# Performance work log

Measured on AMD Instinct MI355X. Metric: run time of the kernel, lower is better.

Reference implementation:

```python
import jax, jax.numpy as jnp
import numpy as np

B, T, D = 32, 128, 64
SPK, CELL, NCLS = 2, 64, 6
DIMS = [300, 74, 35]
BETA = 0.8            # QActivation beta
TWO_PI = 2 * 3.14     # repo uses 2*3.14, not 2*pi


def _unitary(seed, d):
    rng = np.random.default_rng(seed)
    m = rng.normal(size=(d, d)) + 1j * rng.normal(size=(d, d))
    q, _ = np.linalg.qr(m)  # exact unitary -> stable 128-step recurrence
    return jnp.asarray(q.real, jnp.float32), jnp.asarray(q.imag, jnp.float32)


def setup_inputs() -> dict:
    key = jax.random.key(0)
    ks = jax.random.split(key, 16)
    inp = {}
    for i, dm in enumerate(DIMS):
        inp[f"mod{i}"] = jax.random.normal(ks[i], (B, T, dm), jnp.float32)
        inp[f"Wp{i}"] = jax.random.normal(ks[3 + i], (dm, D), jnp.float32) / np.sqrt(dm)
        inp[f"bp{i}"] = jnp.zeros((D,), jnp.float32)
    inp["smask"] = jax.random.uniform(ks[6], (B, T, SPK), dtype=jnp.float32)
    inp["umask"] = jnp.ones((B, T), jnp.float32)
    inp["phase_table"] = jax.random.uniform(ks[7], (SPK, D), dtype=jnp.float32)
    inp["Uh_r"], inp["Uh_i"] = _unitary(1, D)
    inp["Ux_r"], inp["Ux_i"] = _unitary(2, D)
    inp["Lambda"] = jnp.asarray([0.5], jnp.float32)
    inp["K_r"] = jax.random.normal(ks[8], (D, D), jnp.float32) / np.sqrt(D)
    inp["K_i"] = jax.random.normal(ks[9], (D, D), jnp.float32) / np.sqrt(D)
    inp["W1"] = jax.random.normal(ks[10], (D, CELL), jnp.float32) / np.sqrt(D)
    inp["b1"] = jnp.zeros((CELL,), jnp.float32)
    inp["W2"] = jax.random.normal(ks[11], (CELL, NCLS), jnp.float32) / np.sqrt(CELL)
    inp["b2"] = jnp.zeros((NCLS,), jnp.float32)
    return inp


def reference(mod0, mod1, mod2, smask, umask, Wp0, bp0, Wp1, bp1, Wp2, bp2,
              phase_table, Uh_r, Uh_i, Ux_r, Ux_i, Lambda, K_r, K_i, W1, b1, W2, b2):
    d = Uh_r.shape[0]
    b, t = mod0.shape[0], mod0.shape[1]
    mods, Ws, bs = [mod0, mod1, mod2], [Wp0, Wp1, Wp2], [bp0, bp1, bp2]
    # per-modality projections + ReLU -> utterance reps (B,T,D)
    reps = [jax.nn.relu(m @ W + bb) for m, W, bb in zip(mods, Ws, bs)]
    # L2Norm -> softmax mixture weights over modalities (B,T,3)
    norms = jnp.stack([jnp.linalg.norm(r, axis=-1) for r in reps], axis=-1)
    weights = jax.nn.softmax(norms, axis=-1)
    # PositionEmbedding: speaker-conditioned phase + sinusoidal-style frequencies
    sid = jnp.argmax(smask, axis=-1)                                  # (B,T) speaker id
    freq = 1.0 / (10000.0 ** (jnp.arange(d, dtype=jnp.float32) / d))  # (D,)
    pos = jnp.arange(t, dtype=jnp.float32)[None, :, None]             # (1,T,1)
    phase = pos * freq + phase_table[sid] * TWO_PI                    # (B,T,D)
    eiphi = jnp.exp(1j * phase).astype(jnp.complex64)
    # ComplexMultiply + QOuter + QMixture fused: rho = sum_m w_m |psi_m><psi_m|
    rho = jnp.zeros((b, t, d, d), jnp.complex64)
    for m, rep in enumerate(reps):
        amp = rep / jnp.maximum(jnp.linalg.norm(rep, axis=-1, keepdims=True), 1e-12)
        psi = amp.astype(jnp.complex64) * eiphi                       # (B,T,D) pure state
        rho = rho + weights[..., m, None, None].astype(jnp.complex64) * \
              jnp.einsum('bti,btj->btij', psi, psi.conj())
    # QRNNCell recurrence (num_layers=1): h' = lam*Ux rho Ux^H + (1-lam)*Uh h Uh^H
    Uh = (Uh_r + 1j * Uh_i).astype(jnp.complex64)
    Ux = (Ux_r + 1j * Ux_i).astype(jnp.complex64)
    lam = Lambda[0].astype(jnp.complex64)
    mixed_eye = jnp.eye(d, dtype=jnp.complex64) / d

    def step(h, rho_t):
        hx = jnp.einsum('ij,bjk,lk->bil', Ux, rho_t, Ux.conj())
        hh = jnp.einsum('ij,bjk,lk->bil', Uh, h, Uh.conj())
        h_new = lam * hx + (1.0 - lam) * hh
        out = BETA * h_new + (1.0 - BETA) * mixed_eye  # QActivation (trace-preserving)
        return h_new, out

    h0 = jnp.broadcast_to(mixed_eye, (b, d, d))
    _, outs = jax.lax.scan(step, h0, jnp.swapaxes(rho, 0, 1))         # (T,B,D,D)
    rho_out = jnp.swapaxes(outs, 0, 1)                                # (B,T,D,D)
    # QMeasurement: p_j = Re( k_j^H rho k_j )
    K = (K_r + 1j * K_i).astype(jnp.complex64)
    probs = jnp.einsum('jm,btmn,jn->btj', K.conj(), rho_out, K).real  # (B,T,D)
    # SimpleNet head (dropout off in eval) + log_softmax over classes
    h1 = jax.nn.relu(probs @ W1 + b1)
    logits = jnp.tanh(h1 @ W2 + b2)                                   # (B,T,C)
    return jax.nn.log_softmax(logits, axis=2)
```

## Files before the change

kernel.cpp:

```cpp
#include <hip/hip_runtime.h>
#include <hip/hip_bf16.h>
#include <math.h>

#define DD 64
#define TT 128
#define BBATCH 32
#define BT (BBATCH*TT)
#define ND 16
#define BETA_C 0.8f
#define TWO_PI_R 6.28f
#define LG2_10000 13.28771237954945f
#define SW 328

typedef float2 cf;
typedef _Float16 f16;
typedef _Float16 half8 __attribute__((ext_vector_type(8)));
typedef _Float16 half4 __attribute__((ext_vector_type(4)));
typedef float f32x4 __attribute__((ext_vector_type(4)));

__device__ __forceinline__ void cfma(cf& acc, cf a, cf b){
  acc.x = fmaf(a.x, b.x, fmaf(-a.y, b.y, acc.x));
  acc.y = fmaf(a.x, b.y, fmaf( a.y, b.x, acc.y));
}

template<int KDIM, int KPAD>
__device__ __forceinline__ f32x4 prep_phase(
    const float* __restrict__ Wp, const float* __restrict__ modg,
    f16* sWpT, f16* sMod, int tid, int w, int l15, int l4)
{
  __syncthreads();
  constexpr int PAD = KPAD - KDIM;
  for (int i = tid; i < 64*PAD; i += 256) {
    const int r = i / PAD, p = KDIM + (i - r*PAD);
    sWpT[r*SW + p] = (f16)0.f;
  }
  for (int i = tid; i < 16*PAD; i += 256) {
    const int r = i / PAD, p = KDIM + (i - r*PAD);
    sMod[r*SW + p] = (f16)0.f;
  }
  for (int i = tid; i < KDIM*16; i += 256) {
    const int p = i >> 4, c4 = (i & 15) << 2;
    const float4 v = *(const float4*)&Wp[p*64 + c4];
    sWpT[(c4+0)*SW + p] = (f16)v.x;
    sWpT[(c4+1)*SW + p] = (f16)v.y;
    sWpT[(c4+2)*SW + p] = (f16)v.z;
    sWpT[(c4+3)*SW + p] = (f16)v.w;
  }
  for (int i = tid; i < (16*KDIM)/4; i += 256) {
    const float4 v = *(const float4*)&modg[i*4];
    const float vv[4] = {v.x, v.y, v.z, v.w};
    #pragma unroll
    for (int e2 = 0; e2 < 4; ++e2) {
      const int flat = i*4 + e2;
      const int r = flat / KDIM, p = flat - r*KDIM;
      sMod[r*SW + p] = (f16)vv[e2];
    }
  }
  __syncthreads();
  f32x4 acc = {0.f, 0.f, 0.f, 0.f};
  #pragma unroll
  for (int s = 0; s < KPAD/32; ++s) {
    const half8 a = *(const half8*)&sWpT[(w*16 + l15)*SW + s*32 + l4*8];
    const half8 b = *(const half8*)&sMod[l15*SW + s*32 + l4*8];
    acc = __builtin_amdgcn_mfma_f32_16x16x32_f16(a, b, acc, 0, 0, 0);
  }
  return acc;
}

__global__ __launch_bounds__(256) void k_front(
    const float* __restrict__ mod0, const float* __restrict__ Wp0, const float* __restrict__ bp0,
    const float* __restrict__ mod1, const float* __restrict__ Wp1, const float* __restrict__ bp1,
    const float* __restrict__ mod2, const float* __restrict__ Wp2, const float* __restrict__ bp2,
    const float* __restrict__ smask, const float* __restrict__ ptab,
    const float* __restrict__ Uhr, const float* __restrict__ Uhi,
    const float* __restrict__ Uxr, const float* __restrict__ Uxi,
    const float* __restrict__ Kr,  const float* __restrict__ Ki,
    f16* __restrict__ PsiR, f16* __restrict__ PsiI,
    f16* __restrict__ Cre, f16* __restrict__ Cim, f16* __restrict__ Cmn,
    float* __restrict__ kn)
{
  __shared__ __align__(16) char smem[65536];
  const int tid = threadIdx.x, w = tid >> 6, lane = tid & 63;
  const int l15 = lane & 15, l4 = lane >> 4;

  if (blockIdx.x < 64) {
    cf* st = (cf*)smem;
    cf (*red)[64] = (cf(*)[64])(smem + 512);
    const int j = blockIdx.x, c = lane;

    cf uh[16], ux[16];
    #pragma unroll
    for (int i = 0; i < 16; ++i) {
      const int p = w*16 + i;
      uh[i] = make_float2(Uhr[p*64 + c], Uhi[p*64 + c]);
      ux[i] = make_float2(Uxr[p*64 + c], Uxi[p*64 + c]);
    }
    if (w == 0) {
      const cf kj = make_float2(Kr[j*64 + c], -Ki[j*64 + c]);
      st[c] = kj;
      float q = fmaf(kj.x, kj.x, kj.y*kj.y);
      #pragma unroll
      for (int off = 32; off; off >>= 1) q += __shfl_xor(q, off);
      if (c == 0) kn[j] = q;
    }
    __syncthreads();

    for (int D = 0; D < ND; ++D) {
      cf cA = {0.f,0.f}, cB = {0.f,0.f}, tA = {0.f,0.f}, tB = {0.f,0.f};
      #pragma unroll
      for (int i = 0; i < 16; i += 2) {
        const cf t0 = st[w*16 + i], t1 = st[w*16 + i + 1];
        cfma(cA, t0, ux[i]); cfma(cB, t1, ux[i+1]);
        cfma(tA, t0, uh[i]); cfma(tB, t1, uh[i+1]);
      }
      red[w][c]     = make_float2(cA.x + cB.x, cA.y + cB.y);
      red[4 + w][c] = make_float2(tA.x + tB.x, tA.y + tB.y);
      __syncthreads();
      if (w == 0) {
        const cf r0 = red[0][c], r1 = red[1][c], r2 = red[2][c], r3 = red[3][c];
        const float crx = r0.x + r1.x + r2.x + r3.x;
        const float cry = r0.y + r1.y + r2.y + r3.y;
        const size_t row = (size_t)(D*64 + j)*64 + c;
        Cre[row] = (f16)crx;
        Cim[row] = (f16)cry;
        Cmn[row] = (f16)(-cry);
      } else if (w == 1) {
        const cf r0 = red[4][c], r1 = red[5][c], r2 = red[6][c], r3 = red[7][c];
        st[c] = make_float2(r0.x + r1.x + r2.x + r3.x, r0.y + r1.y + r2.y + r3.y);
      }
      __syncthreads();
    }
    return;
  }

  f16* sWpT = (f16*)smem;
  f16* sMod = (f16*)(smem + 41984);
  float* repS = (float*)(smem + 52480);
  const int bt0 = (int)(blockIdx.x - 64) * 16;

  const f32x4 a0 = prep_phase<300,320>(Wp0, mod0 + (size_t)bt0*300, sWpT, sMod, tid, w, l15, l4);
  #pragma unroll
  for (int r = 0; r < 4; ++r) {
    const int d = w*16 + l4*4 + r;
    repS[(0*16 + l15)*68 + d] = a0[r] + bp0[d];
  }
  const f32x4 a1 = prep_phase<74,96>(Wp1, mod1 + (size_t)bt0*74, sWpT, sMod, tid, w, l15, l4);
  #pragma unroll
  for (int r = 0; r < 4; ++r) {
    const int d = w*16 + l4*4 + r;
    repS[(1*16 + l15)*68 + d] = a1[r] + bp1[d];
  }
  const f32x4 a2 = prep_phase<35,64>(Wp2, mod2 + (size_t)bt0*35, sWpT, sMod, tid, w, l15, l4);
  #pragma unroll
  for (int r = 0; r < 4; ++r) {
    const int d = w*16 + l4*4 + r;
    repS[(2*16 + l15)*68 + d] = a2[r] + bp2[d];
  }
  __syncthreads();

  const int btl = tid >> 4, g = tid & 15;
  float4 v0 = *(float4*)&repS[(0*16 + btl)*68 + g*4];
  float4 v1 = *(float4*)&repS[(1*16 + btl)*68 + g*4];
  float4 v2 = *(float4*)&repS[(2*16 + btl)*68 + g*4];
  v0.x = fmaxf(v0.x, 0.f); v0.y = fmaxf(v0.y, 0.f); v0.z = fmaxf(v0.z, 0.f); v0.w = fmaxf(v0.w, 0.f);
  v1.x = fmaxf(v1.x, 0.f); v1.y = fmaxf(v1.y, 0.f); v1.z = fmaxf(v1.z, 0.f); v1.w = fmaxf(v1.w, 0.f);
  v2.x = fmaxf(v2.x, 0.f); v2.y = fmaxf(v2.y, 0.f); v2.z = fmaxf(v2.z, 0.f); v2.w = fmaxf(v2.w, 0.f);

  float q0 = v0.x*v0.x + v0.y*v0.y + v0.z*v0.z + v0.w*v0.w;
  float q1 = v1.x*v1.x + v1.y*v1.y + v1.z*v1.z + v1.w*v1.w;
  float q2 = v2.x*v2.x + v2.y*v2.y + v2.z*v2.z + v2.w*v2.w;
  #pragma unroll
  for (int off = 8; off; off >>= 1) {
    q0 += __shfl_xor(q0, off);
    q1 += __shfl_xor(q1, off);
    q2 += __shfl_xor(q2, off);
  }
  const float n0 = sqrtf(q0), n1 = sqrtf(q1), n2 = sqrtf(q2);
  const float mx = fmaxf(n0, fmaxf(n1, n2));
  const float e0 = expf(n0 - mx), e1 = expf(n1 - mx), e2 = expf(n2 - mx);
  const float inv = 1.f / (e0 + e1 + e2);
  const float sc0 = sqrtf(e0*inv) / fmaxf(n0, 1e-12f);
  const float sc1 = sqrtf(e1*inv) / fmaxf(n1, 1e-12f);
  const float sc2 = sqrtf(e2*inv) / fmaxf(n2, 1e-12f);

  const int btg = bt0 + btl;
  const int t = btg & (TT-1);
  const int sid = (smask[btg*2 + 1] > smask[btg*2]) ? 1 : 0;

  float cs[4], sn[4];
  #pragma unroll
  for (int i = 0; i < 4; ++i) {
    const int d = g*4 + i;
    const float freq = exp2f(-((float)d * (1.f/64.f)) * LG2_10000);
    const float ph = (float)t * freq + ptab[sid*64 + d] * TWO_PI_R;
    sincosf(ph, &sn[i], &cs[i]);
  }
  const float am0[4] = {v0.x*sc0, v0.y*sc0, v0.z*sc0, v0.w*sc0};
  const float am1[4] = {v1.x*sc1, v1.y*sc1, v1.z*sc1, v1.w*sc1};
  const float am2[4] = {v2.x*sc2, v2.y*sc2, v2.z*sc2, v2.w*sc2};
  half4 wr, wi;
  #pragma unroll
  for (int i = 0; i < 4; ++i) { wr[i] = (f16)(am0[i]*cs[i]); wi[i] = (f16)(am0[i]*sn[i]); }
  *(half4*)&PsiR[(size_t)(0*BT + btg)*64 + g*4] = wr;
  *(half4*)&PsiI[(size_t)(0*BT + btg)*64 + g*4] = wi;
  #pragma unroll
  for (int i = 0; i < 4; ++i) { wr[i] = (f16)(am1[i]*cs[i]); wi[i] = (f16)(am1[i]*sn[i]); }
  *(half4*)&PsiR[(size_t)(1*BT + btg)*64 + g*4] = wr;
  *(half4*)&PsiI[(size_t)(1*BT + btg)*64 + g*4] = wi;
  #pragma unroll
  for (int i = 0; i < 4; ++i) { wr[i] = (f16)(am2[i]*cs[i]); wi[i] = (f16)(am2[i]*sn[i]); }
  *(half4*)&PsiR[(size_t)(2*BT + btg)*64 + g*4] = wr;
  *(half4*)&PsiI[(size_t)(2*BT + btg)*64 + g*4] = wi;
}

#define PST 72
__global__ __launch_bounds__(256) void k_E(
    const f16* __restrict__ Cre, const f16* __restrict__ Cim, const f16* __restrict__ Cmn,
    const f16* __restrict__ PsiR, const f16* __restrict__ PsiI,
    float* __restrict__ e)
{
  __shared__ __align__(16) f16 sP[3][2][64][PST];
  const int bsg = blockIdx.x >> 4, cg = blockIdx.x & 15;
  const int tid = threadIdx.x, w = tid >> 6, lane = tid & 63;
  const int l15 = lane & 15, l4 = lane >> 4;

  for (int idx = tid; idx < 512; idx += 256) {
    const int r = idx >> 3, c8 = (idx & 7) << 3;
    #pragma unroll
    for (int k = 0; k < 3; ++k) {
      const size_t g = ((size_t)(k*BT + bsg*64 + r))*64 + c8;
      *(uint4*)&sP[k][0][r][c8] = *(const uint4*)&PsiR[g];
      *(uint4*)&sP[k][1][r][c8] = *(const uint4*)&PsiI[g];
    }
  }

  const size_t arow = ((size_t)(cg*64 + w*16 + l15))*64 + l4*8;
  half8 aRe[2], aIm[2], aMn[2];
  aRe[0] = *(const half8*)&Cre[arow]; aRe[1] = *(const half8*)&Cre[arow + 32];
  aIm[0] = *(const half8*)&Cim[arow]; aIm[1] = *(const half8*)&Cim[arow + 32];
  aMn[0] = *(const half8*)&Cmn[arow]; aMn[1] = *(const half8*)&Cmn[arow + 32];
  __syncthreads();

  #pragma unroll
  for (int ct = 0; ct < 4; ++ct) {
    f32x4 eA = {0.f,0.f,0.f,0.f};
    #pragma unroll
    for (int k = 0; k < 3; ++k) {
      f32x4 xr = {0.f,0.f,0.f,0.f}, xi = {0.f,0.f,0.f,0.f};
      #pragma unroll
      for (int kk = 0; kk < 2; ++kk) {
        const half8 bRe = *(const half8*)&sP[k][0][ct*16 + l15][l4*8 + kk*32];
        const half8 bIm = *(const half8*)&sP[k][1][ct*16 + l15][l4*8 + kk*32];
        xr = __builtin_amdgcn_mfma_f32_16x16x32_f16(aRe[kk], bRe, xr, 0, 0, 0);
        xr = __builtin_amdgcn_mfma_f32_16x16x32_f16(aMn[kk], bIm, xr, 0, 0, 0);
        xi = __builtin_amdgcn_mfma_f32_16x16x32_f16(aRe[kk], bIm, xi, 0, 0, 0);
        xi = __builtin_amdgcn_mfma_f32_16x16x32_f16(aIm[kk], bRe, xi, 0, 0, 0);
      }
      #pragma unroll
      for (int r = 0; r < 4; ++r)
        eA[r] = fmaf(xr[r], xr[r], fmaf(xi[r], xi[r], eA[r]));
    }
    float4 ev = make_float4(eA[0], eA[1], eA[2], eA[3]);
    *(float4*)&e[(size_t)(bsg*64 + ct*16 + l15)*1024 + cg*64 + w*16 + l4*4] = ev;
  }
}

__global__ __launch_bounds__(256) void k_head(const float* __restrict__ e,
    const float* __restrict__ kn, const float* __restrict__ Lam,
    const float* __restrict__ W1, const float* __restrict__ b1,
    const float* __restrict__ W2, const float* __restrict__ b2,
    float* __restrict__ out)
{
  __shared__ float pr[4][64];
  __shared__ float h1[4][64];
  __shared__ float lg[4][6];
  const int q = threadIdx.x >> 6, j = threadIdx.x & 63;
  const int bt = blockIdx.x*4 + q;
  const int b = bt >> 7, t = bt & (TT-1);
  const float lam = Lam[0], om = 1.f - lam;

  float acc = 0.f, wD = BETA_C * lam;
  const int nd = min(ND, t + 1);
  for (int D = 0; D < nd; ++D) {
    acc += wD * e[(size_t)(b*TT + t - D)*1024 + D*64 + j];
    wD *= om;
  }
  const float omt = powf(om, (float)(t + 1));
  acc += (BETA_C*omt + (1.f - BETA_C)) * kn[j] * (1.f/64.f);
  pr[q][j] = acc;
  __syncthreads();

  float a1 = b1[j];
  for (int dd = 0; dd < 64; ++dd) a1 = fmaf(pr[q][dd], W1[dd*64 + j], a1);
  h1[q][j] = fmaxf(a1, 0.f);
  __syncthreads();

  if (j < 6) {
    float a2 = b2[j];
    for (int c = 0; c < 64; ++c) a2 = fmaf(h1[q][c], W2[c*6 + j], a2);
    lg[q][j] = tanhf(a2);
  }
  __syncthreads();
  if (j < 6) {
    float mx = -1e30f;
    #pragma unroll
    for (int n = 0; n < 6; ++n) mx = fmaxf(mx, lg[q][n]);
    float se = 0.f;
    #pragma unroll
    for (int n = 0; n < 6; ++n) se += expf(lg[q][n] - mx);
    out[bt*6 + j] = lg[q][j] - mx - logf(se);
  }
}

extern "C" void kernel_launch(void* const* d_in, const int* in_sizes, int n_in,
                              void* d_out, int out_size, void* d_ws, size_t ws_size,
                              hipStream_t stream)
{
  const float* mod0  = (const float*)d_in[0];
  const float* Wp0   = (const float*)d_in[1];
  const float* bp0   = (const float*)d_in[2];
  const float* mod1  = (const float*)d_in[3];
  const float* Wp1   = (const float*)d_in[4];
  const float* bp1   = (const float*)d_in[5];
  const float* mod2  = (const float*)d_in[6];
  const float* Wp2   = (const float*)d_in[7];
  const float* bp2   = (const float*)d_in[8];
  const float* smask = (const float*)d_in[9];
  const float* ptab  = (const float*)d_in[11];
  const float* Uhr   = (const float*)d_in[12];
  const float* Uhi   = (const float*)d_in[13];
  const float* Uxr   = (const float*)d_in[14];
  const float* Uxi   = (const float*)d_in[15];
  const float* Lam   = (const float*)d_in[16];
  const float* Kr    = (const float*)d_in[17];
  const float* Ki    = (const float*)d_in[18];
  const float* W1    = (const float*)d_in[19];
  const float* b1    = (const float*)d_in[20];
  const float* W2    = (const float*)d_in[21];
  const float* b2    = (const float*)d_in[22];

  char* ws = (char*)d_ws;
  float* kn   = (float*)(ws);
  f16*   Cre  = (f16*)  (ws + ((size_t)1024 << 10));
  f16*   Cim  = (f16*)  (ws + ((size_t)1280 << 10));
  f16*   Cmn  = (f16*)  (ws + ((size_t)1536 << 10));
  f16*   PsiR = (f16*)  (ws + ((size_t)2 << 20));
  f16*   PsiI = (f16*)  (ws + ((size_t)4 << 20));
  float* e    = (float*)(ws + ((size_t)6 << 20));
  if (ws_size < ((size_t)24 << 20)) return;

  k_front<<<320, 256, 0, stream>>>(mod0, Wp0, bp0, mod1, Wp1, bp1, mod2, Wp2, bp2,
                                   smask, ptab, Uhr, Uhi, Uxr, Uxi, Kr, Ki,
                                   PsiR, PsiI, Cre, Cim, Cmn, kn);
  k_E<<<1024, 256, 0, stream>>>(Cre, Cim, Cmn, PsiR, PsiI, e);
  k_head<<<1024, 256, 0, stream>>>(e, kn, Lam, W1, b1, W2, b2, (float*)d_out);
}
```

Measured before the change: 46.76 us.

## Store energy tensor in fp16, halve k_E grid, stage W1 in LDS

Result: no change. 47.00 us (+0.5%).

```diff
diff --git a/kernel.cpp b/kernel.cpp
--- a/kernel.cpp
+++ b/kernel.cpp
@@ -217,10 +217,10 @@
 __global__ __launch_bounds__(256) void k_E(
     const f16* __restrict__ Cre, const f16* __restrict__ Cim, const f16* __restrict__ Cmn,
     const f16* __restrict__ PsiR, const f16* __restrict__ PsiI,
-    float* __restrict__ e)
+    f16* __restrict__ e16)
 {
   __shared__ __align__(16) f16 sP[3][2][64][PST];
-  const int bsg = blockIdx.x >> 4, cg = blockIdx.x & 15;
+  const int bsg = blockIdx.x >> 3, cgg = blockIdx.x & 7;
   const int tid = threadIdx.x, w = tid >> 6, lane = tid & 63;
   const int l15 = lane & 15, l4 = lane >> 4;
 
@@ -233,56 +233,67 @@
       *(uint4*)&sP[k][1][r][c8] = *(const uint4*)&PsiI[g];
     }
   }
-
-  const size_t arow = ((size_t)(cg*64 + w*16 + l15))*64 + l4*8;
-  half8 aRe[2], aIm[2], aMn[2];
-  aRe[0] = *(const half8*)&Cre[arow]; aRe[1] = *(const half8*)&Cre[arow + 32];
-  aIm[0] = *(const half8*)&Cim[arow]; aIm[1] = *(const half8*)&Cim[arow + 32];
-  aMn[0] = *(const half8*)&Cmn[arow]; aMn[1] = *(const half8*)&Cmn[arow + 32];
-  __syncthreads();
-
-  #pragma unroll
-  for (int ct = 0; ct < 4; ++ct) {
-    f32x4 eA = {0.f,0.f,0.f,0.f};
-    #pragma unroll
-    for (int k = 0; k < 3; ++k) {
-      f32x4 xr = {0.f,0.f,0.f,0.f}, xi = {0.f,0.f,0.f,0.f};
+  __syncthreads();
+
+  #pragma unroll
+  for (int cc = 0; cc < 2; ++cc) {
+    const int cg = cgg*2 + cc;
+    const size_t arow = ((size_t)(cg*64 + w*16 + l15))*64 + l4*8;
+    half8 aRe[2], aIm[2], aMn[2];
+    aRe[0] = *(const half8*)&Cre[arow]; aRe[1] = *(const half8*)&Cre[arow + 32];
+    aIm[0] = *(const half8*)&Cim[arow]; aIm[1] = *(const half8*)&Cim[arow + 32];
+    aMn[0] = *(const half8*)&Cmn[arow]; aMn[1] = *(const half8*)&Cmn[arow + 32];
+
+    #pragma unroll
+    for (int ct = 0; ct < 4; ++ct) {
+      f32x4 eA = {0.f,0.f,0.f,0.f};
       #pragma unroll
-      for (int kk = 0; kk < 2; ++kk) {
-        const half8 bRe = *(const half8*)&sP[k][0][ct*16 + l15][l4*8 + kk*32];
-        const half8 bIm = *(const half8*)&sP[k][1][ct*16 + l15][l4*8 + kk*32];
-        xr = __builtin_amdgcn_mfma_f32_16x16x32_f16(aRe[kk], bRe, xr, 0, 0, 0);
-        xr = __builtin_amdgcn_mfma_f32_16x16x32_f16(aMn[kk], bIm, xr, 0, 0, 0);
-        xi = __builtin_amdgcn_mfma_f32_16x16x32_f16(aRe[kk], bIm, xi, 0, 0, 0);
-        xi = __builtin_amdgcn_mfma_f32_16x16x32_f16(aIm[kk], bRe, xi, 0, 0, 0);
+      for (int k = 0; k < 3; ++k) {
+        f32x4 xr = {0.f,0.f,0.f,0.f}, xi = {0.f,0.f,0.f,0.f};
+        #pragma unroll
+        for (int kk = 0; kk < 2; ++kk) {
+          const half8 bRe = *(const half8*)&sP[k][0][ct*16 + l15][l4*8 + kk*32];
+          const half8 bIm = *(const half8*)&sP[k][1][ct*16 + l15][l4*8 + kk*32];
+          xr = __builtin_amdgcn_mfma_f32_16x16x32_f16(aRe[kk], bRe, xr, 0, 0, 0);
+          xr = __builtin_amdgcn_mfma_f32_16x16x32_f16(aMn[kk], bIm, xr, 0, 0, 0);
+          xi = __builtin_amdgcn_mfma_f32_16x16x32_f16(aRe[kk], bIm, xi, 0, 0, 0);
+          xi = __builtin_amdgcn_mfma_f32_16x16x32_f16(aIm[kk], bRe, xi, 0, 0, 0);
+        }
+        #pragma unroll
+        for (int r = 0; r < 4; ++r)
+          eA[r] = fmaf(xr[r], xr[r], fmaf(xi[r], xi[r], eA[r]));
       }
+      half4 ev;
       #pragma unroll
-      for (int r = 0; r < 4; ++r)
-        eA[r] = fmaf(xr[r], xr[r], fmaf(xi[r], xi[r], eA[r]));
-    }
-    float4 ev = make_float4(eA[0], eA[1], eA[2], eA[3]);
-    *(float4*)&e[(size_t)(bsg*64 + ct*16 + l15)*1024 + cg*64 + w*16 + l4*4] = ev;
-  }
-}
-
-__global__ __launch_bounds__(256) void k_head(const float* __restrict__ e,
+      for (int r = 0; r < 4; ++r) ev[r] = (f16)eA[r];
+      *(half4*)&e16[(size_t)(bsg*64 + ct*16 + l15)*1024 + cg*64 + w*16 + l4*4] = ev;
+    }
+  }
+}
+
+__global__ __launch_bounds__(256) void k_head(const f16* __restrict__ e16,
     const float* __restrict__ kn, const float* __restrict__ Lam,
     const float* __restrict__ W1, const float* __restrict__ b1,
     const float* __restrict__ W2, const float* __restrict__ b2,
     float* __restrict__ out)
 {
+  __shared__ float sW1[4096];
   __shared__ float pr[4][64];
   __shared__ float h1[4][64];
   __shared__ float lg[4][6];
-  const int q = threadIdx.x >> 6, j = threadIdx.x & 63;
+  const int tid = threadIdx.x;
+  const int q = tid >> 6, j = tid & 63;
   const int bt = blockIdx.x*4 + q;
   const int b = bt >> 7, t = bt & (TT-1);
   const float lam = Lam[0], om = 1.f - lam;
 
+  for (int i = tid*4; i < 4096; i += 1024)
+    *(float4*)&sW1[i] = *(const float4*)&W1[i];
+
   float acc = 0.f, wD = BETA_C * lam;
   const int nd = min(ND, t + 1);
   for (int D = 0; D < nd; ++D) {
-    acc += wD * e[(size_t)(b*TT + t - D)*1024 + D*64 + j];
+    acc += wD * (float)e16[(size_t)(b*TT + t - D)*1024 + D*64 + j];
     wD *= om;
   }
   const float omt = powf(om, (float)(t + 1));
@@ -291,7 +302,7 @@
   __syncthreads();
 
   float a1 = b1[j];
-  for (int dd = 0; dd < 64; ++dd) a1 = fmaf(pr[q][dd], W1[dd*64 + j], a1);
+  for (int dd = 0; dd < 64; ++dd) a1 = fmaf(pr[q][dd], sW1[dd*64 + j], a1);
   h1[q][j] = fmaxf(a1, 0.f);
   __syncthreads();
 
@@ -346,12 +357,12 @@
   f16*   Cmn  = (f16*)  (ws + ((size_t)1536 << 10));
   f16*   PsiR = (f16*)  (ws + ((size_t)2 << 20));
   f16*   PsiI = (f16*)  (ws + ((size_t)4 << 20));
-  float* e    = (float*)(ws + ((size_t)6 << 20));
-  if (ws_size < ((size_t)24 << 20)) return;
+  f16*   e16  = (f16*)  (ws + ((size_t)6 << 20));
+  if (ws_size < ((size_t)16 << 20)) return;
 
   k_front<<<320, 256, 0, stream>>>(mod0, Wp0, bp0, mod1, Wp1, bp1, mod2, Wp2, bp2,
                                    smask, ptab, Uhr, Uhi, Uxr, Uxi, Kr, Ki,
                                    PsiR, PsiI, Cre, Cim, Cmn, kn);
-  k_E<<<1024, 256, 0, stream>>>(Cre, Cim, Cmn, PsiR, PsiI, e);
-  k_head<<<1024, 256, 0, stream>>>(e, kn, Lam, W1, b1, W2, b2, (float*)d_out);
-}
+  k_E<<<512, 256, 0, stream>>>(Cre, Cim, Cmn, PsiR, PsiI, e16);
+  k_head<<<1024, 256, 0, stream>>>(e16, kn, Lam, W1, b1, W2, b2, (float*)d_out);
+}
```
